# Performance work log

Hardware: AMD Instinct MI355X
Metric: run time of the kernel (lower is better)

The kernel has to match this reference:

```python
import jax, jax.numpy as jnp
import numpy as np


def setup_inputs() -> dict:
    key = jax.random.key(0)
    k1, k2, k3 = jax.random.split(key, 3)
    B, N, C = 8, 4096, 768
    x = jax.random.normal(k1, (B, N, C), dtype=jnp.float32)
    # torch Linear weights, stored transposed so y = x @ W; scaled like trunc-normal init
    w_qkv = jax.random.normal(k2, (C, 3 * C), dtype=jnp.float32) * 0.02
    w_proj = jax.random.normal(k3, (C, C), dtype=jnp.float32) * 0.02
    b_proj = jnp.zeros((C,), dtype=jnp.float32)
    return {"x": x, "w_qkv": w_qkv, "w_proj": w_proj, "b_proj": b_proj, "num_heads": 12}


def reference(x, w_qkv, w_proj, b_proj, num_heads):
    B, N, C = x.shape
    H = num_heads
    D = C // H
    # qkv projection (no bias), split into per-head q/k/v: (B, H, N, D)
    qkv = (x @ w_qkv).reshape(B, N, 3, H, D).transpose(2, 0, 3, 1, 4)
    q, k, v = qkv[0], qkv[1], qkv[2]
    # ELU+1 feature map (positive features)
    q = jax.nn.elu(q) + 1.0
    k = jax.nn.elu(k) + 1.0
    # global kv accumulation: (B, H, D, D)
    kv = jnp.einsum("bhsd,bhse->bhde", k, v)
    # normalizer z: (B, H, N)
    z = 1.0 / jnp.einsum("bhsd,bhd->bhs", q, k.sum(axis=-2))
    # output: (B, H, N, D)
    out = jnp.einsum("bhde,bhsd,bhs->bhse", kv, q, z)
    out = out.transpose(0, 2, 1, 3).reshape(B, N, C)
    out = out @ w_proj + b_proj
    return out, kv
```

## Files before the change

### kernel.cpp

```cpp
#include <hip/hip_runtime.h>
#include <hip/hip_bf16.h>

typedef short bf16x8 __attribute__((ext_vector_type(8)));
typedef float f32x4 __attribute__((ext_vector_type(4)));

#define MFMA_BF16 __builtin_amdgcn_mfma_f32_16x16x32_bf16
#define BARRIER() asm volatile("s_barrier" ::: "memory")

__device__ __forceinline__ float bf2f(short u) {
  return __uint_as_float(((unsigned int)(unsigned short)u) << 16);
}
__device__ __forceinline__ unsigned short f2bf(float f) {
  unsigned int u = __float_as_uint(f);
  u = u + 0x7FFFu + ((u >> 16) & 1u);
  return (unsigned short)(u >> 16);
}

__global__ __launch_bounds__(256)
void cvt_f32_bf16(const float* __restrict__ in, unsigned short* __restrict__ out, int n8) {
  int i = blockIdx.x * 256 + threadIdx.x;
  if (i >= n8) return;
  const float4* p = (const float4*)in + (size_t)i * 2;
  float4 a = p[0], b = p[1];
  bf16x8 o;
  o[0] = (short)f2bf(a.x); o[1] = (short)f2bf(a.y); o[2] = (short)f2bf(a.z); o[3] = (short)f2bf(a.w);
  o[4] = (short)f2bf(b.x); o[5] = (short)f2bf(b.y); o[6] = (short)f2bf(b.z); o[7] = (short)f2bf(b.w);
  *((bf16x8*)out + i) = o;
}

__global__ __launch_bounds__(256)
void tcvt(const float* __restrict__ in, unsigned short* __restrict__ out, int K, int N) {
  __shared__ float t[32][33];
  int n0 = blockIdx.x * 32, k0 = blockIdx.y * 32;
  int tx = threadIdx.x & 31, ty = threadIdx.x >> 5;
#pragma unroll
  for (int j = 0; j < 4; ++j)
    t[ty + 8 * j][tx] = in[(size_t)(k0 + ty + 8 * j) * N + n0 + tx];
  __syncthreads();
#pragma unroll
  for (int j = 0; j < 4; ++j)
    out[(size_t)(n0 + ty + 8 * j) * K + k0 + tx] = f2bf(t[tx][ty + 8 * j]);
}

template <int EPI, int NTILES>
__global__ __launch_bounds__(512, 1)
void gemmP(const unsigned short* __restrict__ A, const unsigned short* __restrict__ Bt,
           void* __restrict__ Cout, const float* __restrict__ bias,
           int N, int K, int eluCols) {
  __shared__ __align__(16) unsigned short lds[77824];
  const int tid = threadIdx.x;
  const int wid = tid >> 6, lane = tid & 63;
  const int wr = wid >> 2, wc = wid & 3;
  const int fr = lane & 15, fq = lane >> 4;
  const int bm = blockIdx.x & 127;
  const int g  = blockIdx.x >> 7;
  const int rowA0 = bm << 8;
  const int bn0 = g * NTILES;

  const int sr  = (wid << 4) + (lane >> 2);
  const int scb = (lane & 3) << 4;
  const int co  = (scb ^ (((sr >> 1) & 3) << 4)) >> 1;
  const int stW = wid << 9;

  int aOff[8], bOff[2];
#pragma unroll
  for (int m = 0; m < 8; ++m) {
    int row = (wr << 7) + (m << 4) + fr;
    aOff[m] = (row << 5) + (((fq << 4) ^ (((row >> 1) & 3) << 4)) >> 1);
  }
#pragma unroll
  for (int n = 0; n < 2; ++n) {
    int row = (wc << 5) + (n << 4) + fr;
    bOff[n] = (row << 5) + (((fq << 4) ^ (((row >> 1) & 3) << 4)) >> 1);
  }

  auto issueA = [&](int slotS, int h, int j, int kcol) {
    const unsigned short* src = A + (size_t)(rowA0 + (j << 7) + sr) * K + kcol + co;
    __builtin_amdgcn_global_load_lds(
        (const __attribute__((address_space(1))) void*)src,
        (__attribute__((address_space(3))) void*)(lds + slotS + (h << 13) + (j << 12) + stW),
        16, 0, 0);
  };
  auto issueB = [&](int slotS, int h, int kcol, int brow0) {
    const unsigned short* src = Bt + (size_t)(brow0 + sr) * K + kcol + co;
    __builtin_amdgcn_global_load_lds(
        (const __attribute__((address_space(1))) void*)src,
        (__attribute__((address_space(3))) void*)(lds + slotS + 16384 + (h << 12) + stW),
        16, 0, 0);
  };

  const int TOTG = NTILES * 12;
#pragma unroll
  for (int G = 0; G < 2; ++G) {
#pragma unroll
    for (int h = 0; h < 2; ++h) {
      int kcol = (G << 6) + (h << 5);
      issueA(G * 24576, h, 0, kcol);
      issueA(G * 24576, h, 1, kcol);
      issueB(G * 24576, h, kcol, bn0 << 7);
    }
  }

  int ktn = 2, bnn = bn0, sn = 2;
  int G = 0, slotS = 0;
  const size_t ldc = (size_t)N;

  for (int T = 0; T < NTILES; ++T) {
    f32x4 acc[8][2];
#pragma unroll
    for (int m = 0; m < 8; ++m) { acc[m][0] = (f32x4)(0.f); acc[m][1] = (f32x4)(0.f); }

    for (int kt = 0; kt < 12; ++kt) {
#pragma unroll
      for (int h = 0; h < 2; ++h) {
        if (G < TOTG - 2)            { asm volatile("s_waitcnt vmcnt(9)" ::: "memory"); }
        else if (G == TOTG - 2) { if (h == 0) asm volatile("s_waitcnt vmcnt(9)" ::: "memory");
                                  else        asm volatile("s_waitcnt vmcnt(6)" ::: "memory"); }
        else                    { if (h == 0) asm volatile("s_waitcnt vmcnt(3)" ::: "memory");
                                  else        asm volatile("s_waitcnt vmcnt(0)" ::: "memory"); }
        BARRIER();
        const unsigned short* sA = lds + slotS + (h << 13);
        const unsigned short* sB = lds + slotS + 16384 + (h << 12);
        bf16x8 av[8];
#pragma unroll
        for (int m = 0; m < 8; ++m) av[m] = *(const bf16x8*)(sA + aOff[m]);
        bf16x8 b0 = *(const bf16x8*)(sB + bOff[0]);
        bf16x8 b1 = *(const bf16x8*)(sB + bOff[1]);
        if (G + 2 < TOTG) {
          int ss = sn * 24576;
          int kcol = (ktn << 6) + (h << 5);
          issueA(ss, h, 0, kcol);
          issueA(ss, h, 1, kcol);
          issueB(ss, h, kcol, bnn << 7);
        }
        __builtin_amdgcn_s_setprio(1);
#pragma unroll
        for (int m = 0; m < 8; ++m) acc[m][0] = MFMA_BF16(av[m], b0, acc[m][0], 0, 0, 0);
#pragma unroll
        for (int m = 0; m < 8; ++m) acc[m][1] = MFMA_BF16(av[m], b1, acc[m][1], 0, 0, 0);
        __builtin_amdgcn_s_setprio(0);
      }
      ++G;
      if (++ktn == 12) { ktn = 0; ++bnn; }
      if (++sn == 3) sn = 0;
      slotS += 24576; if (slotS == 73728) slotS = 0;
    }

    {
      unsigned short* sp = lds + 73728 + (wid << 9);
      const int bnT = bn0 + T;
      const int colBase = (bnT << 7) + (wc << 5);
      const size_t gr0 = (size_t)rowA0 + ((size_t)wr << 7);
      if (EPI == 0) {
        unsigned short* Cb = (unsigned short*)Cout;
#pragma unroll
        for (int m = 0; m < 8; ++m) {
#pragma unroll
          for (int n = 0; n < 2; ++n) {
            int col = colBase + (n << 4) + fr;
            bool elu = col < eluCols;
#pragma unroll
            for (int r = 0; r < 4; ++r) {
              float x = acc[m][n][r];
              if (elu) x = x > 0.f ? x + 1.f : __expf(x);
              sp[(((fq << 2) + r) << 5) + (n << 4) + fr] = f2bf(x);
            }
          }
          asm volatile("s_waitcnt lgkmcnt(0)" ::: "memory");
          __builtin_amdgcn_sched_barrier(0);
          bf16x8 v = *(const bf16x8*)(sp + (lane << 3));
          *(bf16x8*)(Cb + (gr0 + (m << 4) + (lane >> 2)) * ldc + colBase + ((lane & 3) << 3)) = v;
          asm volatile("s_waitcnt lgkmcnt(0)" ::: "memory");
          __builtin_amdgcn_sched_barrier(0);
        }
      } else {
        float* Cf = (float*)Cout;
        float* spf = (float*)sp;
        float bv[2];
#pragma unroll
        for (int n = 0; n < 2; ++n) bv[n] = bias[colBase + (n << 4) + fr];
#pragma unroll
        for (int m = 0; m < 8; ++m) {
#pragma unroll
          for (int n = 0; n < 2; ++n) {
#pragma unroll
            for (int r = 0; r < 4; ++r)
              spf[(((fq << 2) + r) << 4) + fr] = acc[m][n][r] + bv[n];
            asm volatile("s_waitcnt lgkmcnt(0)" ::: "memory");
            __builtin_amdgcn_sched_barrier(0);
            f32x4 v = *(const f32x4*)(spf + (lane << 2));
            *(f32x4*)(Cf + (gr0 + (m << 4) + (lane >> 2)) * ldc + colBase + (n << 4) + ((lane & 3) << 2)) = v;
            asm volatile("s_waitcnt lgkmcnt(0)" ::: "memory");
            __builtin_amdgcn_sched_barrier(0);
          }
        }
      }
    }
  }
}

__global__ __launch_bounds__(256)
void kv_accum(const unsigned short* __restrict__ qkv, float* __restrict__ kv_out,
              float* __restrict__ ksum) {
  const int bh = blockIdx.x;
  const int b = bh / 12, h = bh - b * 12;
  const int s0 = blockIdx.y * 512;
  __shared__ __align__(16) float ks[128][64];
  __shared__ __align__(16) float vs[128][64];
  const int td = threadIdx.x >> 4, te = threadIdx.x & 15;
  float acc[4][4] = {};
  float ksl[4] = {};
  for (int c = 0; c < 4; ++c) {
    const size_t rowbase = (size_t)(b * 4096 + s0 + c * 128) * 2304;
    const unsigned short* kg = qkv + rowbase + 768 + h * 64;
    const unsigned short* vg = qkv + rowbase + 1536 + h * 64;
    for (int i = threadIdx.x; i < 128 * 8; i += 256) {
      int s = i >> 3, dc = (i & 7) << 3;
      bf16x8 k8 = *(const bf16x8*)(kg + (size_t)s * 2304 + dc);
      bf16x8 v8 = *(const bf16x8*)(vg + (size_t)s * 2304 + dc);
#pragma unroll
      for (int j = 0; j < 8; ++j) {
        ks[s][dc + j] = bf2f(k8[j]);
        vs[s][dc + j] = bf2f(v8[j]);
      }
    }
    __syncthreads();
#pragma unroll 4
    for (int s = 0; s < 128; ++s) {
      f32x4 ka = *(const f32x4*)&ks[s][td * 4];
      f32x4 va = *(const f32x4*)&vs[s][te * 4];
#pragma unroll
      for (int i = 0; i < 4; ++i) {
        ksl[i] += ka[i];
#pragma unroll
        for (int j = 0; j < 4; ++j) acc[i][j] += ka[i] * va[j];
      }
    }
    __syncthreads();
  }
  float* kvp = kv_out + ((size_t)bh * 64 + td * 4) * 64 + te * 4;
#pragma unroll
  for (int i = 0; i < 4; ++i)
#pragma unroll
    for (int j = 0; j < 4; ++j) atomicAdd(&kvp[(size_t)i * 64 + j], acc[i][j]);
  if (te == 0) {
#pragma unroll
    for (int i = 0; i < 4; ++i) atomicAdd(&ksum[bh * 64 + td * 4 + i], ksl[i]);
  }
}

__global__ __launch_bounds__(256)
void attn_out(const unsigned short* __restrict__ qkv, const float* __restrict__ kv,
              const float* __restrict__ ksum, unsigned short* __restrict__ attn) {
  const int bh = blockIdx.x;
  const int b = bh / 12, h = bh - b * 12;
  const int s0 = blockIdx.y * 64;
  __shared__ __align__(16) float kvs[64][64];
  __shared__ float kss[64];
  {
    const float4* kvg = (const float4*)(kv + (size_t)bh * 4096);
    float4* kvl = (float4*)&kvs[0][0];
    for (int i = threadIdx.x; i < 1024; i += 256) kvl[i] = kvg[i];
    if (threadIdx.x < 64) kss[threadIdx.x] = ksum[bh * 64 + threadIdx.x];
  }
  __syncthreads();
  const int tr = threadIdx.x >> 2;
  const int te = threadIdx.x & 3;
  const int s = s0 + tr;
  const unsigned short* qg = qkv + (size_t)(b * 4096 + s) * 2304 + h * 64;
  bf16x8 q8[8];
#pragma unroll
  for (int c = 0; c < 8; ++c) q8[c] = *(const bf16x8*)(qg + c * 8);
  float acc[16] = {};
  float zz = 0.f;
#pragma unroll
  for (int c = 0; c < 8; ++c) {
#pragma unroll
    for (int j = 0; j < 8; ++j) {
      const int d = c * 8 + j;
      const float qd = bf2f(q8[c][j]);
      zz += qd * kss[d];
      const f32x4* kvr = (const f32x4*)&kvs[d][te * 16];
#pragma unroll
      for (int q4 = 0; q4 < 4; ++q4) {
        f32x4 kk = kvr[q4];
        acc[q4 * 4 + 0] += qd * kk[0];
        acc[q4 * 4 + 1] += qd * kk[1];
        acc[q4 * 4 + 2] += qd * kk[2];
        acc[q4 * 4 + 3] += qd * kk[3];
      }
    }
  }
  const float z = 1.f / zz;
  bf16x8 o0, o1;
#pragma unroll
  for (int j = 0; j < 8; ++j) o0[j] = (short)f2bf(acc[j] * z);
#pragma unroll
  for (int j = 0; j < 8; ++j) o1[j] = (short)f2bf(acc[8 + j] * z);
  unsigned short* og = attn + (size_t)(b * 4096 + s) * 768 + h * 64 + te * 16;
  *(bf16x8*)og = o0;
  *(bf16x8*)(og + 8) = o1;
}

extern "C" void kernel_launch(void* const* d_in, const int* in_sizes, int n_in,
                              void* d_out, int out_size, void* d_ws, size_t ws_size,
                              hipStream_t stream) {
  const float* x      = (const float*)d_in[0];
  const float* w_qkv  = (const float*)d_in[1];
  const float* w_proj = (const float*)d_in[2];
  const float* b_proj = (const float*)d_in[3];
  const int B = 8, N = 4096, C = 768, H = 12, D = 64;
  const int M = B * N;
  const int N1 = 3 * C;

  char* ws = (char*)d_ws;
  unsigned short* xb     = (unsigned short*)(ws);
  unsigned short* wqkvT  = (unsigned short*)(ws + 50331648);
  unsigned short* wprojT = (unsigned short*)(ws + 53870592);
  float*          ksum   = (float*)(ws + 55050240);
  unsigned short* qkvb   = (unsigned short*)(ws + 55074816);

  float* out_main = (float*)d_out;
  float* kv_out   = out_main + (size_t)M * C;

  hipMemsetAsync(kv_out, 0, (size_t)B * H * D * D * sizeof(float), stream);
  hipMemsetAsync(ksum, 0, (size_t)B * H * D * sizeof(float), stream);

  cvt_f32_bf16<<<(M * C / 8 + 255) / 256, 256, 0, stream>>>(x, xb, M * C / 8);
  tcvt<<<dim3(N1 / 32, C / 32), 256, 0, stream>>>(w_qkv, wqkvT, C, N1);
  tcvt<<<dim3(C / 32, C / 32), 256, 0, stream>>>(w_proj, wprojT, C, C);

  gemmP<0, 9><<<256, 512, 0, stream>>>(xb, wqkvT, qkvb, nullptr, N1, C, 2 * C);

  kv_accum<<<dim3(B * H, N / 512), 256, 0, stream>>>(qkvb, kv_out, ksum);

  attn_out<<<dim3(B * H, N / 64), 256, 0, stream>>>(qkvb, kv_out, ksum, xb);

  gemmP<1, 3><<<256, 512, 0, stream>>>(xb, wprojT, d_out, b_proj, C, C, 0);
}
```

Baseline: 517.5 us.

## Retile persistent GEMM to 128x128 blocks with 256 threads, two per CU

Replaces the 512-thread, 256x128-tile persistent GEMM with a 256-thread kernel using 128x128 output tiles, 4 waves each computing 64x64, and a 4-slot LDS ring with K-step 32 and 3-deep prefetch. Launches 512 blocks with launch bounds allowing 2 blocks per CU, aiming for better occupancy and latency hiding with smaller LDS per block. Each wave now does 4x4 MFMAs per step, giving a more balanced A/B register reuse. The trade-off is lower per-block A reuse (smaller M tile) and more global loads overall.

Result: slower. 548.7 us (+6.0%).

```diff
diff --git a/kernel.cpp b/kernel.cpp
--- a/kernel.cpp
+++ b/kernel.cpp
@@ -43,153 +43,155 @@
 }
 
 template <int EPI, int NTILES>
-__global__ __launch_bounds__(512, 1)
-void gemmP(const unsigned short* __restrict__ A, const unsigned short* __restrict__ Bt,
-           void* __restrict__ Cout, const float* __restrict__ bias,
-           int N, int K, int eluCols) {
-  __shared__ __align__(16) unsigned short lds[77824];
+__global__ __launch_bounds__(256, 2)
+void gemmP2(const unsigned short* __restrict__ A, const unsigned short* __restrict__ Bt,
+            void* __restrict__ Cout, const float* __restrict__ bias,
+            int N, int K, int eluCols) {
+  __shared__ __align__(16) unsigned short lds[36864];
   const int tid = threadIdx.x;
   const int wid = tid >> 6, lane = tid & 63;
-  const int wr = wid >> 2, wc = wid & 3;
+  const int wr = wid >> 1, wc = wid & 1;
   const int fr = lane & 15, fq = lane >> 4;
-  const int bm = blockIdx.x & 127;
-  const int g  = blockIdx.x >> 7;
-  const int rowA0 = bm << 8;
-  const int bn0 = g * NTILES;
-
-  const int sr  = (wid << 4) + (lane >> 2);
-  const int scb = (lane & 3) << 4;
+  const int stripe = blockIdx.x & 255;
+  const int half = blockIdx.x >> 8;
+  const int rowA0 = stripe << 7;
+  const int bn0 = half * NTILES;
+
+  const int sr  = tid >> 2;
+  const int scb = (tid & 3) << 4;
   const int co  = (scb ^ (((sr >> 1) & 3) << 4)) >> 1;
   const int stW = wid << 9;
 
-  int aOff[8], bOff[2];
-#pragma unroll
-  for (int m = 0; m < 8; ++m) {
-    int row = (wr << 7) + (m << 4) + fr;
+  int aOff[4], bOff[4];
+#pragma unroll
+  for (int m = 0; m < 4; ++m) {
+    int row = (wr << 6) + (m << 4) + fr;
     aOff[m] = (row << 5) + (((fq << 4) ^ (((row >> 1) & 3) << 4)) >> 1);
   }
 #pragma unroll
-  for (int n = 0; n < 2; ++n) {
-    int row = (wc << 5) + (n << 4) + fr;
-    bOff[n] = (row << 5) + (((fq << 4) ^ (((row >> 1) & 3) << 4)) >> 1);
-  }
-
-  auto issueA = [&](int slotS, int h, int j, int kcol) {
-    const unsigned short* src = A + (size_t)(rowA0 + (j << 7) + sr) * K + kcol + co;
+  for (int n = 0; n < 4; ++n) {
+    int row = (wc << 6) + (n << 4) + fr;
+    bOff[n] = 4096 + (row << 5) + (((fq << 4) ^ (((row >> 1) & 3) << 4)) >> 1);
+  }
+
+  auto issueA = [&](int slotS, int j, int kcol) {
+    const unsigned short* src = A + (size_t)(rowA0 + (j << 6) + sr) * K + kcol + co;
     __builtin_amdgcn_global_load_lds(
         (const __attribute__((address_space(1))) void*)src,
-        (__attribute__((address_space(3))) void*)(lds + slotS + (h << 13) + (j << 12) + stW),
+        (__attribute__((address_space(3))) void*)(lds + slotS + (j << 11) + stW),
         16, 0, 0);
   };
-  auto issueB = [&](int slotS, int h, int kcol, int brow0) {
-    const unsigned short* src = Bt + (size_t)(brow0 + sr) * K + kcol + co;
+  auto issueB = [&](int slotS, int j, int kcol, int brow0) {
+    const unsigned short* src = Bt + (size_t)(brow0 + (j << 6) + sr) * K + kcol + co;
     __builtin_amdgcn_global_load_lds(
         (const __attribute__((address_space(1))) void*)src,
-        (__attribute__((address_space(3))) void*)(lds + slotS + 16384 + (h << 12) + stW),
+        (__attribute__((address_space(3))) void*)(lds + slotS + 4096 + (j << 11) + stW),
         16, 0, 0);
   };
 
-  const int TOTG = NTILES * 12;
-#pragma unroll
-  for (int G = 0; G < 2; ++G) {
-#pragma unroll
-    for (int h = 0; h < 2; ++h) {
-      int kcol = (G << 6) + (h << 5);
-      issueA(G * 24576, h, 0, kcol);
-      issueA(G * 24576, h, 1, kcol);
-      issueB(G * 24576, h, kcol, bn0 << 7);
-    }
-  }
-
-  int ktn = 2, bnn = bn0, sn = 2;
-  int G = 0, slotS = 0;
+  const int TOTG = NTILES * 24;
+#pragma unroll
+  for (int g = 0; g < 3; ++g) {
+    int kcol = g << 5;
+    int ss = g << 13;
+    issueA(ss, 0, kcol); issueA(ss, 1, kcol);
+    issueB(ss, 0, kcol, bn0 << 7); issueB(ss, 1, kcol, bn0 << 7);
+  }
+
+  int G = 0, ktn = 3, bnn = bn0;
   const size_t ldc = (size_t)N;
 
   for (int T = 0; T < NTILES; ++T) {
-    f32x4 acc[8][2];
-#pragma unroll
-    for (int m = 0; m < 8; ++m) { acc[m][0] = (f32x4)(0.f); acc[m][1] = (f32x4)(0.f); }
-
-    for (int kt = 0; kt < 12; ++kt) {
-#pragma unroll
-      for (int h = 0; h < 2; ++h) {
-        if (G < TOTG - 2)            { asm volatile("s_waitcnt vmcnt(9)" ::: "memory"); }
-        else if (G == TOTG - 2) { if (h == 0) asm volatile("s_waitcnt vmcnt(9)" ::: "memory");
-                                  else        asm volatile("s_waitcnt vmcnt(6)" ::: "memory"); }
-        else                    { if (h == 0) asm volatile("s_waitcnt vmcnt(3)" ::: "memory");
-                                  else        asm volatile("s_waitcnt vmcnt(0)" ::: "memory"); }
-        BARRIER();
-        const unsigned short* sA = lds + slotS + (h << 13);
-        const unsigned short* sB = lds + slotS + 16384 + (h << 12);
-        bf16x8 av[8];
-#pragma unroll
-        for (int m = 0; m < 8; ++m) av[m] = *(const bf16x8*)(sA + aOff[m]);
-        bf16x8 b0 = *(const bf16x8*)(sB + bOff[0]);
-        bf16x8 b1 = *(const bf16x8*)(sB + bOff[1]);
-        if (G + 2 < TOTG) {
-          int ss = sn * 24576;
-          int kcol = (ktn << 6) + (h << 5);
-          issueA(ss, h, 0, kcol);
-          issueA(ss, h, 1, kcol);
-          issueB(ss, h, kcol, bnn << 7);
-        }
-        __builtin_amdgcn_s_setprio(1);
-#pragma unroll
-        for (int m = 0; m < 8; ++m) acc[m][0] = MFMA_BF16(av[m], b0, acc[m][0], 0, 0, 0);
-#pragma unroll
-        for (int m = 0; m < 8; ++m) acc[m][1] = MFMA_BF16(av[m], b1, acc[m][1], 0, 0, 0);
-        __builtin_amdgcn_s_setprio(0);
-      }
+    f32x4 acc[4][4];
+#pragma unroll
+    for (int m = 0; m < 4; ++m)
+#pragma unroll
+      for (int n = 0; n < 4; ++n) acc[m][n] = (f32x4)(0.f);
+
+    for (int kt = 0; kt < 24; ++kt) {
+      if (G < TOTG - 2)       { asm volatile("s_waitcnt vmcnt(8)" ::: "memory"); }
+      else if (G == TOTG - 2) { asm volatile("s_waitcnt vmcnt(4)" ::: "memory"); }
+      else                    { asm volatile("s_waitcnt vmcnt(0)" ::: "memory"); }
+      BARRIER();
+      const unsigned short* sl = lds + ((G & 3) << 13);
+      bf16x8 av[4], bw[4];
+#pragma unroll
+      for (int m = 0; m < 4; ++m) av[m] = *(const bf16x8*)(sl + aOff[m]);
+#pragma unroll
+      for (int n = 0; n < 4; ++n) bw[n] = *(const bf16x8*)(sl + bOff[n]);
+      if (G + 3 < TOTG) {
+        int ss = ((G + 3) & 3) << 13;
+        int kcol = ktn << 5;
+        issueA(ss, 0, kcol); issueA(ss, 1, kcol);
+        issueB(ss, 0, kcol, bnn << 7); issueB(ss, 1, kcol, bnn << 7);
+      }
+      __builtin_amdgcn_s_setprio(1);
+#pragma unroll
+      for (int m = 0; m < 4; ++m)
+#pragma unroll
+        for (int n = 0; n < 4; ++n)
+          acc[m][n] = MFMA_BF16(av[m], bw[n], acc[m][n], 0, 0, 0);
+      __builtin_amdgcn_s_setprio(0);
       ++G;
-      if (++ktn == 12) { ktn = 0; ++bnn; }
-      if (++sn == 3) sn = 0;
-      slotS += 24576; if (slotS == 73728) slotS = 0;
+      if (++ktn == 24) { ktn = 0; ++bnn; }
     }
 
     {
-      unsigned short* sp = lds + 73728 + (wid << 9);
       const int bnT = bn0 + T;
-      const int colBase = (bnT << 7) + (wc << 5);
-      const size_t gr0 = (size_t)rowA0 + ((size_t)wr << 7);
+      const int colBase = (bnT << 7) + (wc << 6);
+      const size_t gr0 = (size_t)rowA0 + ((size_t)wr << 6);
       if (EPI == 0) {
+        unsigned short* sp = lds + 32768 + (wid << 10);
         unsigned short* Cb = (unsigned short*)Cout;
 #pragma unroll
-        for (int m = 0; m < 8; ++m) {
-#pragma unroll
-          for (int n = 0; n < 2; ++n) {
+        for (int m = 0; m < 4; ++m) {
+#pragma unroll
+          for (int n = 0; n < 4; ++n) {
             int col = colBase + (n << 4) + fr;
             bool elu = col < eluCols;
 #pragma unroll
             for (int r = 0; r < 4; ++r) {
               float x = acc[m][n][r];
               if (elu) x = x > 0.f ? x + 1.f : __expf(x);
-              sp[(((fq << 2) + r) << 5) + (n << 4) + fr] = f2bf(x);
+              sp[(((fq << 2) + r) << 6) + (n << 4) + fr] = f2bf(x);
             }
           }
           asm volatile("s_waitcnt lgkmcnt(0)" ::: "memory");
           __builtin_amdgcn_sched_barrier(0);
-          bf16x8 v = *(const bf16x8*)(sp + (lane << 3));
-          *(bf16x8*)(Cb + (gr0 + (m << 4) + (lane >> 2)) * ldc + colBase + ((lane & 3) << 3)) = v;
+          int row = lane >> 2, cg = lane & 3;
+          bf16x8 v0 = *(const bf16x8*)(sp + (row << 6) + (cg << 4));
+          bf16x8 v1 = *(const bf16x8*)(sp + (row << 6) + (cg << 4) + 8);
+          unsigned short* dst = Cb + (gr0 + (m << 4) + row) * ldc + colBase + (cg << 4);
+          *(bf16x8*)dst = v0;
+          *(bf16x8*)(dst + 8) = v1;
           asm volatile("s_waitcnt lgkmcnt(0)" ::: "memory");
           __builtin_amdgcn_sched_barrier(0);
         }
       } else {
+        float* spf = (float*)(lds + 32768 + (wid << 10));
         float* Cf = (float*)Cout;
-        float* spf = (float*)sp;
-        float bv[2];
-#pragma unroll
-        for (int n = 0; n < 2; ++n) bv[n] = bias[colBase + (n << 4) + fr];
-#pragma unroll
-        for (int m = 0; m < 8; ++m) {
-#pragma unroll
-          for (int n = 0; n < 2; ++n) {
-#pragma unroll
-            for (int r = 0; r < 4; ++r)
-              spf[(((fq << 2) + r) << 4) + fr] = acc[m][n][r] + bv[n];
+        float bv[4];
+#pragma unroll
+        for (int n = 0; n < 4; ++n) bv[n] = bias[colBase + (n << 4) + fr];
+#pragma unroll
+        for (int m = 0; m < 4; ++m) {
+#pragma unroll
+          for (int nh = 0; nh < 2; ++nh) {
+#pragma unroll
+            for (int nn = 0; nn < 2; ++nn) {
+              int n = nh * 2 + nn;
+#pragma unroll
+              for (int r = 0; r < 4; ++r)
+                spf[(((fq << 2) + r) << 5) + (nn << 4) + fr] = acc[m][n][r] + bv[n];
+            }
             asm volatile("s_waitcnt lgkmcnt(0)" ::: "memory");
             __builtin_amdgcn_sched_barrier(0);
-            f32x4 v = *(const f32x4*)(spf + (lane << 2));
-            *(f32x4*)(Cf + (gr0 + (m << 4) + (lane >> 2)) * ldc + colBase + (n << 4) + ((lane & 3) << 2)) = v;
+            int row = lane >> 2, cg = lane & 3;
+            f32x4 v0 = *(const f32x4*)(spf + (row << 5) + (cg << 3));
+            f32x4 v1 = *(const f32x4*)(spf + (row << 5) + (cg << 3) + 4);
+            float* dst = Cf + (gr0 + (m << 4) + row) * ldc + colBase + (nh << 5) + (cg << 3);
+            *(f32x4*)dst = v0;
+            *(f32x4*)(dst + 4) = v1;
             asm volatile("s_waitcnt lgkmcnt(0)" ::: "memory");
             __builtin_amdgcn_sched_barrier(0);
           }
@@ -330,11 +332,11 @@
   tcvt<<<dim3(N1 / 32, C / 32), 256, 0, stream>>>(w_qkv, wqkvT, C, N1);
   tcvt<<<dim3(C / 32, C / 32), 256, 0, stream>>>(w_proj, wprojT, C, C);
 
-  gemmP<0, 9><<<256, 512, 0, stream>>>(xb, wqkvT, qkvb, nullptr, N1, C, 2 * C);
+  gemmP2<0, 9><<<512, 256, 0, stream>>>(xb, wqkvT, qkvb, nullptr, N1, C, 2 * C);
 
   kv_accum<<<dim3(B * H, N / 512), 256, 0, stream>>>(qkvb, kv_out, ksum);
 
   attn_out<<<dim3(B * H, N / 64), 256, 0, stream>>>(qkvb, kv_out, ksum, xb);
 
-  gemmP<1, 3><<<256, 512, 0, stream>>>(xb, wprojT, d_out, b_proj, C, C, 0);
-}
+  gemmP2<1, 3><<<512, 256, 0, stream>>>(xb, wprojT, d_out, b_proj, C, C, 0);
+}
```
